# Performance work log

Measured on AMD Instinct MI355X. Metric: run time of the kernel, lower is better.

The kernel has to match this reference:

```python
import jax, jax.numpy as jnp
import numpy as np

K = 2          # diffusion steps
HID = 64       # hidden_dim
T_OUT = 12     # decoder horizon
EPS = 1e-6


def _random_walk(A):
    # W_fwd = D_out^{-1} A ; W_bwd = D_in^{-1} A^T  (row-normalized)
    W_fwd = A / (A.sum(axis=1, keepdims=True) + EPS)
    AT = A.T
    W_bwd = AT / (AT.sum(axis=1, keepdims=True) + EPS)
    return W_fwd, W_bwd


def _dconv(xin, Wf, Wb, W, b):
    # xin: (B, N, F). K forward + K backward random-walk hops, concat, linear.
    outs = [xin]
    xf = xin
    for _ in range(K):
        xf = jnp.einsum('ij,bjf->bif', Wf, xf)
        outs.append(xf)
    xb = xin
    for _ in range(K):
        xb = jnp.einsum('ij,bjf->bif', Wb, xb)
        outs.append(xb)
    return jnp.concatenate(outs, axis=-1) @ W + b


def _cell(xl, h, Wr, br, Wz, bz, Wn, bn, Wf, Wb):
    xh = jnp.concatenate([xl, h], axis=-1)
    r = jax.nn.sigmoid(_dconv(xh, Wf, Wb, Wr, br))
    z = jax.nn.sigmoid(_dconv(xh, Wf, Wb, Wz, bz))
    xrh = jnp.concatenate([xl, r * h], axis=-1)
    n = jnp.tanh(_dconv(xrh, Wf, Wb, Wn, bn))
    return (1.0 - z) * h + z * n


def setup_inputs() -> dict:
    key = jax.random.key(0)
    ks = jax.random.split(key, 20)
    B, T_in, N = 16, 12, 512
    x = jax.random.normal(ks[0], (B, T_in, N), dtype=jnp.float32)
    A = jax.random.uniform(ks[1], (N, N), dtype=jnp.float32)

    def lin(k, fan_in, fan_out):
        s = 1.0 / np.sqrt(fan_in)
        kw, kb = jax.random.split(k)
        W = jax.random.uniform(kw, (fan_in, fan_out), jnp.float32, -s, s)
        b = jax.random.uniform(kb, (fan_out,), jnp.float32, -s, s)
        return W, b

    in0 = (2 * K + 1) * (1 + HID)    # 325
    in1 = (2 * K + 1) * (2 * HID)    # 640
    Wr0, br0 = lin(ks[2], in0, HID)
    Wz0, bz0 = lin(ks[3], in0, HID)
    Wn0, bn0 = lin(ks[4], in0, HID)
    Wr1, br1 = lin(ks[5], in1, HID)
    Wz1, bz1 = lin(ks[6], in1, HID)
    Wn1, bn1 = lin(ks[7], in1, HID)
    Wp, bp = lin(ks[8], HID, 1)
    return dict(x=x, A=A, Wr0=Wr0, br0=br0, Wz0=Wz0, bz0=bz0, Wn0=Wn0, bn0=bn0,
                Wr1=Wr1, br1=br1, Wz1=Wz1, bz1=bz1, Wn1=Wn1, bn1=bn1, Wp=Wp, bp=bp)


def reference(x, A, Wr0, br0, Wz0, bz0, Wn0, bn0,
              Wr1, br1, Wz1, bz1, Wn1, bn1, Wp, bp):
    Wf, Wb = _random_walk(A)
    B, T_in, N = x.shape
    x4 = x[..., None]                             # (B, T_in, N, 1)
    h0 = jnp.zeros((B, N, HID), x.dtype)
    h1 = jnp.zeros((B, N, HID), x.dtype)

    def enc_step(carry, xt):
        h0, h1 = carry
        h0 = _cell(xt, h0, Wr0, br0, Wz0, bz0, Wn0, bn0, Wf, Wb)
        h1 = _cell(h0, h1, Wr1, br1, Wz1, bz1, Wn1, bn1, Wf, Wb)
        return (h0, h1), None

    (h0, h1), _ = jax.lax.scan(enc_step, (h0, h1), jnp.moveaxis(x4, 1, 0))

    def dec_step(carry, _):
        h0, h1, di = carry
        h0 = _cell(di, h0, Wr0, br0, Wz0, bz0, Wn0, bn0, Wf, Wb)
        h1 = _cell(h0, h1, Wr1, br1, Wz1, bz1, Wn1, bn1, Wf, Wb)
        yt = h1 @ Wp + bp                          # (B, N, 1)
        return (h0, h1, yt), yt

    (_, _, _), ys = jax.lax.scan(dec_step, (h0, h1, x4[:, -1]), None, length=T_OUT)
    return jnp.moveaxis(ys, 0, 1)[..., 0]          # (B, T_out, N)
```

## Files before the change

kernel.cpp:

```cpp
#include <hip/hip_runtime.h>
#include <math.h>

#define T_IN   12
#define T_OUT  12
#define NB     8192
#define EPSV   1e-6f

typedef __attribute__((ext_vector_type(8))) short short8;
typedef __attribute__((ext_vector_type(4))) float floatx4;

__device__ __forceinline__ unsigned short f2bf(float x) {
    union { float f; unsigned u; } v; v.f = x;
    unsigned r = v.u + 0x7fffu + ((v.u >> 16) & 1u);
    return (unsigned short)(r >> 16);
}
__device__ __forceinline__ float bf2f(unsigned short h) {
    union { float f; unsigned u; } v; v.u = ((unsigned)h) << 16;
    return v.f;
}
__device__ __forceinline__ unsigned packbf(float v) {
    unsigned u = __float_as_uint(v);
    unsigned hu = u & 0xffff0000u;
    float r = v - __uint_as_float(hu);
    unsigned ru = __float_as_uint(r);
    return (ru & 0xffff0000u) | (u >> 16);
}
__device__ __forceinline__ void split2(float v, short& h, short& l) {
    unsigned u = __float_as_uint(v);
    h = (short)(u >> 16);
    float r = v - __uint_as_float(u & 0xffff0000u);
    l = (short)(__float_as_uint(r) >> 16);
}

__device__ __forceinline__ float sigmoid_fast(float x) {
    return 1.0f / (1.0f + __expf(-x));
}
__device__ __forceinline__ float tanh_fast(float x) {
    float e = __expf(2.0f * x);
    return 1.0f - 2.0f / (e + 1.0f);
}

struct HopA {
    const float* M[4];
    float* dst0[4];
};

struct HopM {
    const unsigned short* Ahi[4]; const unsigned short* Alo[4];
    const unsigned* src0; const unsigned* src1;
    unsigned* dst0[4]; unsigned* dst1[4];
    int tiles0;
};

struct XHopM {
    const unsigned short* Ahi[4]; const unsigned short* Alo[4];
    const float* X;
    float* Y;
    int ncols;
};

struct WPack { const float* w[4]; unsigned short* hi[4]; unsigned short* lo[4]; };

struct Setup {
    const float* A; float* Wf; float* Wb;
    const float* x; float* xenc;
    const float* W[6]; unsigned short* hi[6]; unsigned short* lo[6];
};

struct LinJob {
    const unsigned* seg[10]; int nseg;
    const float* sx[5]; int sxrow[5]; int nsx;
    const unsigned short* Wh[2]; const unsigned short* Wl[2];
    const float* WO[2]; const float* bias[2];
    const float* h; unsigned* GP; float* Z;
    float* PR;
    int mode;
};

struct NJob {
    const unsigned* seg[10]; int nseg; int ksplit;
    const float* sx[5]; int sxrow[5]; int nsx;
    const unsigned short* Wh; const unsigned short* Wl;
    const float* WO; const float* bias;
    const float* Zb; const float* hin; float* hout; unsigned* hPout;
    int doProj; const float* Wp; const float* bp; float* out; float* di; int t;
};

struct F0 {
    const float* M[4];
    const float* di;
    const float* PR;
    const float* WO[2]; const float* bias[2];
    const float* h0;
    unsigned* GP0; float* Z0; float* HXS;
};

__global__ __launch_bounds__(256) void setup_kernel(Setup s) {
    __shared__ float s1[256], s2[256];
    int bx = blockIdx.x;
    int t = threadIdx.x;
    if (bx < 512) {
        int i = bx;
        float a = s.A[i * 512 + t] + s.A[i * 512 + t + 256];
        float b = s.A[t * 512 + i] + s.A[(t + 256) * 512 + i];
        s1[t] = a; s2[t] = b;
        __syncthreads();
        for (int off = 128; off > 0; off >>= 1) {
            if (t < off) { s1[t] += s1[t + off]; s2[t] += s2[t + off]; }
            __syncthreads();
        }
        float irs = 1.0f / (s1[0] + EPSV);
        float ics = 1.0f / (s2[0] + EPSV);
        for (int j = t; j < 512; j += 256) {
            s.Wf[i * 512 + j] = s.A[i * 512 + j] * irs;
            s.Wb[i * 512 + j] = s.A[j * 512 + i] * ics;
        }
    } else if (bx < 896) {
        int idx = (bx - 512) * 256 + t;
        int j = idx & 511;
        int b = (idx >> 9) & 15;
        int tt = idx >> 13;
        s.xenc[tt * NB + j * 16 + b] = s.x[(b * T_IN + tt) * 512 + j];
    } else {
        int bx2 = bx - 896;
        int g = bx2 / 160;
        int nseg = (g < 3) ? 5 : 10;
        int idx = (bx2 % 160) * 256 + t;
        if (idx < nseg * 4096) {
            int j = idx & 7, ln = (idx >> 3) & 15, ntl = (idx >> 7) & 3, O = idx >> 9;
            int sg = O >> 3, o8 = O & 7;
            int base = (g < 3) ? (65 * sg + 1) : (64 * sg);
            int row = base + o8 * 8 + j;
            int col = ntl * 16 + ln;
            float v = s.W[g][(size_t)row * 64 + col];
            unsigned short h = f2bf(v);
            s.hi[g][idx] = h;
            s.lo[g][idx] = f2bf(v - bf2f(h));
        }
    }
}

__global__ __launch_bounds__(256) void ghop_kernel(HopA a) {
    int z = blockIdx.z;
    const float* Wm = a.M[z];
    const float* X = Wm;
    float* Y = a.dst0[z];
    int col0 = blockIdx.x * 64;
    int row0 = blockIdx.y * 64;
    int tid = threadIdx.x;
    int tx = tid & 15, ty = tid >> 4;
    int kkA = tid & 15, rrA = tid >> 4;
    int ccB = tid & 63, kkB = tid >> 6;

    __shared__ float As[16][68], Bs[16][68];
    float acc[4][4] = {};

    const float* wp = Wm + (row0 + rrA) * 512 + kkA;
    const float* xp = X + (size_t)(col0 + ccB) + (size_t)kkB * 512;

    float ra[4], rb[4];
#pragma unroll
    for (int p = 0; p < 4; ++p) ra[p] = wp[p * 16 * 512];
#pragma unroll
    for (int p = 0; p < 4; ++p) rb[p] = xp[(size_t)(p * 4) * 512];

    for (int k0 = 0; k0 < 512; k0 += 16) {
#pragma unroll
        for (int p = 0; p < 4; ++p) As[kkA][rrA + p * 16] = ra[p];
#pragma unroll
        for (int p = 0; p < 4; ++p) Bs[kkB + p * 4][ccB] = rb[p];
        __syncthreads();
        if (k0 + 16 < 512) {
            int kn = k0 + 16;
#pragma unroll
            for (int p = 0; p < 4; ++p) ra[p] = wp[p * 16 * 512 + kn];
#pragma unroll
            for (int p = 0; p < 4; ++p) rb[p] = xp[(size_t)(kn + p * 4) * 512];
        }
#pragma unroll
        for (int k = 0; k < 16; ++k) {
            const float4 a4 = *(const float4*)&As[k][ty * 4];
            const float4 b4 = *(const float4*)&Bs[k][tx * 4];
            float av[4] = { a4.x, a4.y, a4.z, a4.w };
            float bv[4] = { b4.x, b4.y, b4.z, b4.w };
#pragma unroll
            for (int i = 0; i < 4; ++i)
#pragma unroll
                for (int j = 0; j < 4; ++j)
                    acc[i][j] = fmaf(av[i], bv[j], acc[i][j]);
        }
        __syncthreads();
    }

    int colw = col0 + tx * 4;
#pragma unroll
    for (int i = 0; i < 4; ++i) {
        int row = row0 + ty * 4 + i;
        *(float4*)&Y[(size_t)row * 512 + colw] =
            make_float4(acc[i][0], acc[i][1], acc[i][2], acc[i][3]);
    }
}

__global__ void wpack_kernel(WPack a) {
    int z = blockIdx.y;
    int idx = blockIdx.x * 256 + threadIdx.x;
    int m = idx >> 9, k = idx & 511;
    float x = a.w[z][idx];
    unsigned short h = f2bf(x);
    unsigned short l = f2bf(x - bf2f(h));
    int p = (((m >> 4) * 64 + (k >> 3)) * 16 + (m & 15)) * 8 + (k & 7);
    a.hi[z][p] = h;
    a.lo[z][p] = l;
}

template<int MI>
__global__ __launch_bounds__(256) void hop_mfma(HopM a) {
    int z = blockIdx.z;
    int nt = blockIdx.x;
    const unsigned* X; unsigned* Y; int c0;
    if (nt < a.tiles0) { X = a.src0; Y = a.dst0[z]; c0 = nt * 64; }
    else { X = a.src1; Y = a.dst1[z]; c0 = (nt - a.tiles0) * 64; }
    const unsigned short* Ahi = a.Ahi[z];
    const unsigned short* Alo = a.Alo[z];
    int bm = blockIdx.y * (MI * 32);

    __shared__ unsigned short Bhi_s[2][64][40];
    __shared__ unsigned short Blo_s[2][64][40];

    int tid = threadIdx.x;
    int lane = tid & 63, w = tid >> 6;
    int wm = (w & 1) * (MI * 16), wn = (w >> 1) * 32;
    int ln = lane & 15, quad = lane >> 4;
    int sc = tid & 63, skh = tid >> 6;

    floatx4 acc[MI][2];
#pragma unroll
    for (int mi = 0; mi < MI; ++mi)
#pragma unroll
        for (int ci = 0; ci < 2; ++ci) acc[mi][ci] = (floatx4)0.0f;

    const unsigned* xbase = X + c0 + sc;
    int mtb = (bm + wm) >> 4;

    unsigned uv[8];
#pragma unroll
    for (int j = 0; j < 8; ++j)
        uv[j] = xbase[(size_t)(skh * 8 + j) * 1024];
    {
        short8 h8, l8;
#pragma unroll
        for (int j = 0; j < 8; ++j) {
            h8[j] = (short)(uv[j] & 0xffffu);
            l8[j] = (short)(uv[j] >> 16);
        }
        *(short8*)&Bhi_s[0][sc][skh * 8] = h8;
        *(short8*)&Blo_s[0][sc][skh * 8] = l8;
    }
#pragma unroll
    for (int j = 0; j < 8; ++j)
        uv[j] = xbase[(size_t)(32 + skh * 8 + j) * 1024];

    for (int it = 0; it < 16; ++it) {
        __syncthreads();
        int cur = it & 1;
        if (it + 1 < 16) {
            short8 h8, l8;
#pragma unroll
            for (int j = 0; j < 8; ++j) {
                h8[j] = (short)(uv[j] & 0xffffu);
                l8[j] = (short)(uv[j] >> 16);
            }
            *(short8*)&Bhi_s[cur ^ 1][sc][skh * 8] = h8;
            *(short8*)&Blo_s[cur ^ 1][sc][skh * 8] = l8;
        }
        if (it + 2 < 16) {
            int kn = (it + 2) * 32;
#pragma unroll
            for (int j = 0; j < 8; ++j)
                uv[j] = xbase[(size_t)(kn + skh * 8 + j) * 1024];
        }
        short8 bh[2], bl[2];
#pragma unroll
        for (int ci = 0; ci < 2; ++ci) {
            bh[ci] = *(const short8*)&Bhi_s[cur][wn + ci * 16 + ln][quad * 8];
            bl[ci] = *(const short8*)&Blo_s[cur][wn + ci * 16 + ln][quad * 8];
        }
        int kob = it * 4 + quad;
#pragma unroll
        for (int mi = 0; mi < MI; ++mi) {
            size_t aoff = ((size_t)((mtb + mi) * 64 + kob) * 16 + ln) * 8;
            short8 Ah = *(const short8*)(Ahi + aoff);
            short8 Al = *(const short8*)(Alo + aoff);
#pragma unroll
            for (int ci = 0; ci < 2; ++ci) {
                acc[mi][ci] = __builtin_amdgcn_mfma_f32_16x16x32_bf16(Ah, bh[ci], acc[mi][ci], 0, 0, 0);
                acc[mi][ci] = __builtin_amdgcn_mfma_f32_16x16x32_bf16(Ah, bl[ci], acc[mi][ci], 0, 0, 0);
                acc[mi][ci] = __builtin_amdgcn_mfma_f32_16x16x32_bf16(Al, bh[ci], acc[mi][ci], 0, 0, 0);
            }
        }
    }

#pragma unroll
    for (int mi = 0; mi < MI; ++mi) {
#pragma unroll
        for (int ci = 0; ci < 2; ++ci) {
            int mrow = bm + wm + mi * 16 + quad * 4;
            int col = c0 + wn + ci * 16 + ln;
#pragma unroll
            for (int r = 0; r < 4; ++r)
                Y[(size_t)(mrow + r) * 1024 + col] = packbf(acc[mi][ci][r]);
        }
    }
}

__global__ __launch_bounds__(256) void xhop_mfma(XHopM a) {
    int z = blockIdx.z;
    int c0 = blockIdx.x * 64;
    const unsigned short* Ahi = a.Ahi[z];
    const unsigned short* Alo = a.Alo[z];
    int bm = blockIdx.y * 64;

    __shared__ unsigned short Bhi_s[2][64][40];
    __shared__ unsigned short Blo_s[2][64][40];

    int tid = threadIdx.x;
    int lane = tid & 63, w = tid >> 6;
    int wm = (w & 1) * 32, wn = (w >> 1) * 32;
    int ln = lane & 15, quad = lane >> 4;
    int sc = tid & 63, skh = tid >> 6;

    floatx4 acc[2][2];
#pragma unroll
    for (int mi = 0; mi < 2; ++mi)
#pragma unroll
        for (int ci = 0; ci < 2; ++ci) acc[mi][ci] = (floatx4)0.0f;

    int colS = c0 + sc;
    bool ok = colS < a.ncols;
    const float* xb = a.X + (size_t)(colS >> 4) * NB + (colS & 15);
    int mtb = (bm + wm) >> 4;

    float xv[8];
#pragma unroll
    for (int j = 0; j < 8; ++j)
        xv[j] = ok ? xb[(size_t)(skh * 8 + j) * 16] : 0.0f;
    {
        short8 h8, l8;
#pragma unroll
        for (int j = 0; j < 8; ++j) { short h, l; split2(xv[j], h, l); h8[j] = h; l8[j] = l; }
        *(short8*)&Bhi_s[0][sc][skh * 8] = h8;
        *(short8*)&Blo_s[0][sc][skh * 8] = l8;
    }
#pragma unroll
    for (int j = 0; j < 8; ++j)
        xv[j] = ok ? xb[(size_t)(32 + skh * 8 + j) * 16] : 0.0f;

    for (int it = 0; it < 16; ++it) {
        __syncthreads();
        int cur = it & 1;
        if (it + 1 < 16) {
            short8 h8, l8;
#pragma unroll
            for (int j = 0; j < 8; ++j) { short h, l; split2(xv[j], h, l); h8[j] = h; l8[j] = l; }
            *(short8*)&Bhi_s[cur ^ 1][sc][skh * 8] = h8;
            *(short8*)&Blo_s[cur ^ 1][sc][skh * 8] = l8;
        }
        if (it + 2 < 16) {
            int kn = (it + 2) * 32;
#pragma unroll
            for (int j = 0; j < 8; ++j)
                xv[j] = ok ? xb[(size_t)(kn + skh * 8 + j) * 16] : 0.0f;
        }
        short8 bh[2], bl[2];
#pragma unroll
        for (int ci = 0; ci < 2; ++ci) {
            bh[ci] = *(const short8*)&Bhi_s[cur][wn + ci * 16 + ln][quad * 8];
            bl[ci] = *(const short8*)&Blo_s[cur][wn + ci * 16 + ln][quad * 8];
        }
        int kob = it * 4 + quad;
#pragma unroll
        for (int mi = 0; mi < 2; ++mi) {
            size_t aoff = ((size_t)((mtb + mi) * 64 + kob) * 16 + ln) * 8;
            short8 Ah = *(const short8*)(Ahi + aoff);
            short8 Al = *(const short8*)(Alo + aoff);
#pragma unroll
            for (int ci = 0; ci < 2; ++ci) {
                acc[mi][ci] = __builtin_amdgcn_mfma_f32_16x16x32_bf16(Ah, bh[ci], acc[mi][ci], 0, 0, 0);
                acc[mi][ci] = __builtin_amdgcn_mfma_f32_16x16x32_bf16(Ah, bl[ci], acc[mi][ci], 0, 0, 0);
                acc[mi][ci] = __builtin_amdgcn_mfma_f32_16x16x32_bf16(Al, bh[ci], acc[mi][ci], 0, 0, 0);
            }
        }
    }

#pragma unroll
    for (int mi = 0; mi < 2; ++mi) {
#pragma unroll
        for (int ci = 0; ci < 2; ++ci) {
            int col = c0 + wn + ci * 16 + ln;
            if (col < a.ncols) {
                int mrow = bm + wm + mi * 16 + quad * 4;
                float* yb = a.Y + (size_t)((col >> 4) * 4 + z) * NB + (col & 15);
#pragma unroll
                for (int r = 0; r < 4; ++r)
                    yb[(size_t)(mrow + r) * 16] = acc[mi][ci][r];
            }
        }
    }
}

__device__ __forceinline__ void lin_core2(const unsigned* const* segs, int nseg, int s0,
        const unsigned short* __restrict__ Bh, const unsigned short* __restrict__ Bl,
        int row0, int ln, int quad, int cihalf, floatx4 acc[2]) {
    for (int s = 0; s < nseg; ++s) {
        const unsigned* ap = segs[s] + (size_t)(row0 + ln) * 64 + quad * 8;
#pragma unroll
        for (int hh = 0; hh < 2; ++hh) {
            unsigned u[8];
            *(uint4*)&u[0] = *(const uint4*)(ap + hh * 32);
            *(uint4*)&u[4] = *(const uint4*)(ap + hh * 32 + 4);
            short8 Ah, Al;
#pragma unroll
            for (int j = 0; j < 8; ++j) {
                Ah[j] = (short)(u[j] & 0xffffu);
                Al[j] = (short)(u[j] >> 16);
            }
            int O = (s0 + s) * 8 + hh * 4 + quad;
#pragma unroll
            for (int ci = 0; ci < 2; ++ci) {
                int c_abs = cihalf * 2 + ci;
                size_t boff = ((size_t)(O * 4 + c_abs) * 16 + ln) * 8;
                short8 B1 = *(const short8*)(Bh + boff);
                short8 B2 = *(const short8*)(Bl + boff);
                acc[ci] = __builtin_amdgcn_mfma_f32_16x16x32_bf16(Ah, B1, acc[ci], 0, 0, 0);
                acc[ci] = __builtin_amdgcn_mfma_f32_16x16x32_bf16(Al, B1, acc[ci], 0, 0, 0);
                acc[ci] = __builtin_amdgcn_mfma_f32_16x16x32_bf16(Ah, B2, acc[ci], 0, 0, 0);
            }
        }
    }
}

__device__ __forceinline__ void lin_scalar2p(const float* const* sx, const int* sxrow,
        int nsx, const float* __restrict__ WO,
        int row0, int ln, int quad, int cihalf, floatx4 acc[2]) {
    for (int t = 0; t < nsx; ++t) {
        const float* wr = WO + (size_t)sxrow[t] * 64;
        const float* sv = sx[t] + row0 + quad * 4;
#pragma unroll
        for (int rr = 0; rr < 4; ++rr) {
            float v = sv[rr];
#pragma unroll
            for (int ci = 0; ci < 2; ++ci)
                acc[ci][rr] = fmaf(v, wr[(cihalf * 2 + ci) * 16 + ln], acc[ci][rr]);
        }
    }
}

__device__ __forceinline__ void rz_body(const LinJob& J, int bx) {
    int w = threadIdx.x >> 6, lane = threadIdx.x & 63;
    int ln = lane & 15, quad = lane >> 4;
    int row0 = bx * 64 + w * 16;
    int gate = blockIdx.y;
    int cihalf = blockIdx.z;
    floatx4 acc[2];
    acc[0] = (floatx4)0.0f; acc[1] = (floatx4)0.0f;
    lin_core2(J.seg, J.nseg, 0, J.Wh[gate], J.Wl[gate], row0, ln, quad, cihalf, acc);
    if (J.nsx) lin_scalar2p(J.sx, J.sxrow, J.nsx, J.WO[gate], row0, ln, quad, cihalf, acc);
    if (J.mode == 0) {
        const float* bias = J.bias[gate];
#pragma unroll
        for (int ci = 0; ci < 2; ++ci) {
            int col = (cihalf * 2 + ci) * 16 + ln;
            float bv = bias[col];
#pragma unroll
            for (int rr = 0; rr < 4; ++rr) {
                int row = row0 + quad * 4 + rr;
                size_t idx = (size_t)row * 64 + col;
                float sg = sigmoid_fast(acc[ci][rr] + bv);
                if (gate == 0) J.GP[idx] = packbf(sg * J.h[idx]);
                else J.Z[idx] = sg;
            }
        }
    } else {
        float* PRg = J.PR + (size_t)gate * ((size_t)NB * 64);
#pragma unroll
        for (int ci = 0; ci < 2; ++ci) {
            int col = (cihalf * 2 + ci) * 16 + ln;
#pragma unroll
            for (int rr = 0; rr < 4; ++rr) {
                int row = row0 + quad * 4 + rr;
                PRg[(size_t)row * 64 + col] = acc[ci][rr];
            }
        }
    }
}

__global__ __launch_bounds__(256) void lin_rz2(LinJob j0, LinJob j1, int xsplit) {
    if ((int)blockIdx.x >= xsplit) rz_body(j1, (int)blockIdx.x - xsplit);
    else                           rz_body(j0, (int)blockIdx.x);
}

__device__ __forceinline__ void n_body(const NJob& J, int bx) {
    int w = threadIdx.x >> 6, lane = threadIdx.x & 63;
    int ln = lane & 15, quad = lane >> 4;
    int kh = w & 1, cihalf = w >> 1;
    int row0 = bx * 16;
    __shared__ float part[2][2][16][17];
    __shared__ float pr[2][16];
    floatx4 acc[2];
    acc[0] = (floatx4)0.0f; acc[1] = (floatx4)0.0f;
    if (kh == 0) {
        lin_core2(J.seg, J.ksplit, 0, J.Wh, J.Wl, row0, ln, quad, cihalf, acc);
    } else {
        lin_core2(J.seg + J.ksplit, J.nseg - J.ksplit, J.ksplit, J.Wh, J.Wl,
                  row0, ln, quad, cihalf, acc);
        if (J.nsx) lin_scalar2p(J.sx, J.sxrow, J.nsx, J.WO, row0, ln, quad, cihalf, acc);
#pragma unroll
        for (int ci = 0; ci < 2; ++ci)
#pragma unroll
            for (int rr = 0; rr < 4; ++rr)
                part[cihalf][ci][quad * 4 + rr][ln] = acc[ci][rr];
    }
    __syncthreads();
    float p[4] = {0.0f, 0.0f, 0.0f, 0.0f};
    if (kh == 0) {
#pragma unroll
        for (int ci = 0; ci < 2; ++ci) {
            int col = (cihalf * 2 + ci) * 16 + ln;
            float bv = J.bias[col];
            float wpv = J.doProj ? J.Wp[col] : 0.0f;
#pragma unroll
            for (int rr = 0; rr < 4; ++rr) {
                int row = row0 + quad * 4 + rr;
                size_t idx = (size_t)row * 64 + col;
                float pre = acc[ci][rr] + part[cihalf][ci][quad * 4 + rr][ln] + bv;
                float nn = tanh_fast(pre);
                float z = J.Zb[idx];
                float hv = J.hin[idx];
                float o = (1.0f - z) * hv + z * nn;
                J.hout[idx] = o;
                J.hPout[idx] = packbf(o);
                p[rr] = fmaf(o, wpv, p[rr]);
            }
        }
        if (J.doProj) {
#pragma unroll
            for (int rr = 0; rr < 4; ++rr) {
                p[rr] += __shfl_xor(p[rr], 1, 64);
                p[rr] += __shfl_xor(p[rr], 2, 64);
                p[rr] += __shfl_xor(p[rr], 4, 64);
                p[rr] += __shfl_xor(p[rr], 8, 64);
            }
            if (ln == 0) {
#pragma unroll
                for (int rr = 0; rr < 4; ++rr)
                    pr[cihalf][quad * 4 + rr] = p[rr];
            }
        }
    }
    __syncthreads();
    if (J.doProj && kh == 0 && cihalf == 0 && ln == 0) {
        float bpv = J.bp[0];
#pragma unroll
        for (int rr = 0; rr < 4; ++rr) {
            int qr = quad * 4 + rr;
            int row = row0 + qr;
            float y = pr[0][qr] + pr[1][qr] + bpv;
            int n = row >> 4, b = row & 15;
            J.out[(b * T_OUT + J.t) * 512 + n] = y;
            J.di[row] = y;
        }
    }
}

__global__ __launch_bounds__(256) void lin_n2(NJob j0, NJob j1, int xsplit) {
    if ((int)blockIdx.x >= xsplit) n_body(j1, (int)blockIdx.x - xsplit);
    else                           n_body(j0, (int)blockIdx.x);
}

__global__ __launch_bounds__(256) void finish0_kernel(F0 a) {
    int n = blockIdx.x;
    int tid = threadIdx.x;
    __shared__ float hopS[4][16];
    __shared__ float sdi[16];

    int g = tid >> 2;
    int sub = tid & 3;
    int m = g >> 4, b = g & 15;
    const float* wrow = a.M[m] + (size_t)n * 512 + sub * 128;
    const float* dv = a.di + (size_t)(sub * 128) * 16 + b;
    float s0 = 0.0f, s1 = 0.0f, s2 = 0.0f, s3 = 0.0f;
#pragma unroll 8
    for (int k = 0; k < 128; k += 4) {
        float4 w4 = *(const float4*)&wrow[k];
        s0 = fmaf(w4.x, dv[(k + 0) * 16], s0);
        s1 = fmaf(w4.y, dv[(k + 1) * 16], s1);
        s2 = fmaf(w4.z, dv[(k + 2) * 16], s2);
        s3 = fmaf(w4.w, dv[(k + 3) * 16], s3);
    }
    float sv = (s0 + s1) + (s2 + s3);
    sv += __shfl_xor(sv, 1, 64);
    sv += __shfl_xor(sv, 2, 64);
    if (sub == 0) {
        hopS[m][b] = sv;
        a.HXS[(size_t)m * NB + n * 16 + b] = sv;
    }
    if (tid < 16) sdi[tid] = a.di[n * 16 + tid];
    __syncthreads();

    int gate = tid >> 7, col = tid & 63, rh = (tid >> 6) & 1;
    const float* WOg = a.WO[gate];
    float w0c = WOg[col];
    float wmc[4];
#pragma unroll
    for (int mm = 0; mm < 4; ++mm)
        wmc[mm] = WOg[(size_t)(65 * (mm + 1)) * 64 + col];
    float bv = a.bias[gate][col];
    const float* PRg = a.PR + (size_t)gate * ((size_t)NB * 64);
#pragma unroll
    for (int rr = 0; rr < 8; ++rr) {
        int bl = rh * 8 + rr;
        int row = n * 16 + bl;
        size_t idx = (size_t)row * 64 + col;
        float pre = PRg[idx] + bv + sdi[bl] * w0c;
#pragma unroll
        for (int mm = 0; mm < 4; ++mm)
            pre = fmaf(hopS[mm][bl], wmc[mm], pre);
        float sg = sigmoid_fast(pre);
        if (gate == 0) a.GP0[idx] = packbf(sg * a.h0[idx]);
        else a.Z0[idx] = sg;
    }
}

extern "C" void kernel_launch(void* const* d_in, const int* in_sizes, int n_in,
                              void* d_out, int out_size, void* d_ws, size_t ws_size,
                              hipStream_t stream) {
    (void)in_sizes; (void)n_in; (void)out_size; (void)ws_size;
    const float* x   = (const float*)d_in[0];
    const float* A   = (const float*)d_in[1];
    const float* Wr0 = (const float*)d_in[2];  const float* br0 = (const float*)d_in[3];
    const float* Wz0 = (const float*)d_in[4];  const float* bz0 = (const float*)d_in[5];
    const float* Wn0 = (const float*)d_in[6];  const float* bn0 = (const float*)d_in[7];
    const float* Wr1 = (const float*)d_in[8];  const float* br1 = (const float*)d_in[9];
    const float* Wz1 = (const float*)d_in[10]; const float* bz1 = (const float*)d_in[11];
    const float* Wn1 = (const float*)d_in[12]; const float* bn1 = (const float*)d_in[13];
    const float* Wp  = (const float*)d_in[14]; const float* bp  = (const float*)d_in[15];
    float* out = (float*)d_out;

    float* ws = (float*)d_ws;
    size_t off = 0;
    auto alloc = [&](size_t nf) { float* p = ws + off; off += nf; return p; };
    const size_t NB64 = (size_t)NB * 64;
    float* Wf  = alloc(262144); float* Wb  = alloc(262144);
    float* W2f = alloc(262144); float* W2b = alloc(262144);
    float* xenc = alloc((size_t)T_IN * NB);
    unsigned short* Whi[4]; unsigned short* Wlo[4];
    for (int m = 0; m < 4; ++m) Whi[m] = (unsigned short*)alloc(131072);
    for (int m = 0; m < 4; ++m) Wlo[m] = (unsigned short*)alloc(131072);
    float* zbase = alloc(12 * NB64);
    float* h0x[2]; unsigned* h0Px[2];
    h0x[1]  = zbase;
    h0Px[1] = (unsigned*)(zbase + NB64);
    float* h1 = zbase + 2 * NB64;
    unsigned* h1P = (unsigned*)(zbase + 3 * NB64);
    unsigned* HAall = (unsigned*)(zbase + 4 * NB64);
    unsigned* HBall = (unsigned*)(zbase + 8 * NB64);
    unsigned* HA[4]; unsigned* HB[4]; unsigned* HG0[4]; unsigned* HG1[4];
    for (int m = 0; m < 4; ++m) HA[m] = HAall + m * NB64;
    for (int m = 0; m < 4; ++m) HB[m] = HBall + m * NB64;
    for (int m = 0; m < 4; ++m) HG0[m] = (unsigned*)alloc(NB64);
    for (int m = 0; m < 4; ++m) HG1[m] = (unsigned*)alloc(NB64);
    unsigned* GP0 = (unsigned*)alloc(NB64);
    unsigned* GP1 = (unsigned*)alloc(NB64);
    float* Z0 = alloc(NB64);
    float* Z1 = alloc(NB64);
    h0x[0]  = alloc(NB64);
    h0Px[0] = (unsigned*)alloc(NB64);
    float* PR0 = alloc(2 * NB64);
    float* XHE = alloc((size_t)T_IN * 4 * NB);
    float* HXSdec = alloc(4 * NB);
    float* di = alloc(NB);
    unsigned short* LWh[6]; unsigned short* LWl[6];
    for (int g = 0; g < 3; ++g) { LWh[g] = (unsigned short*)alloc(10240); LWl[g] = (unsigned short*)alloc(10240); }
    for (int g = 3; g < 6; ++g) { LWh[g] = (unsigned short*)alloc(20480); LWl[g] = (unsigned short*)alloc(20480); }

    hipMemsetAsync(zbase, 0, 12 * NB64 * 4, stream);

    {
        Setup s;
        s.A = A; s.Wf = Wf; s.Wb = Wb;
        s.x = x; s.xenc = xenc;
        const float* WG[6] = { Wr0, Wz0, Wn0, Wr1, Wz1, Wn1 };
        for (int g = 0; g < 6; ++g) { s.W[g] = WG[g]; s.hi[g] = LWh[g]; s.lo[g] = LWl[g]; }
        setup_kernel<<<dim3(1856), 256, 0, stream>>>(s);
    }
    {
        HopA w2 = {};
        w2.M[0] = Wf; w2.M[1] = Wb;
        w2.dst0[0] = W2f; w2.dst0[1] = W2b;
        ghop_kernel<<<dim3(8, 8, 2), 256, 0, stream>>>(w2);
    }
    {
        WPack p;
        p.w[0] = Wf; p.w[1] = W2f; p.w[2] = Wb; p.w[3] = W2b;
        for (int m = 0; m < 4; ++m) { p.hi[m] = Whi[m]; p.lo[m] = Wlo[m]; }
        wpack_kernel<<<dim3(1024, 4), 256, 0, stream>>>(p);
    }
    {
        XHopM xa = {};
        for (int m = 0; m < 4; ++m) { xa.Ahi[m] = Whi[m]; xa.Alo[m] = Wlo[m]; }
        xa.X = xenc; xa.Y = XHE; xa.ncols = 192;
        xhop_mfma<<<dim3(3, 8, 4), 256, 0, stream>>>(xa);
    }

    auto hopSingle = [&](const unsigned* s0, unsigned* const* d0) {
        HopM a = {};
        for (int m = 0; m < 4; ++m) { a.Ahi[m] = Whi[m]; a.Alo[m] = Wlo[m]; }
        a.src0 = s0; a.tiles0 = 16;
        for (int m = 0; m < 4; ++m) a.dst0[m] = d0[m];
        hop_mfma<1><<<dim3(16, 16, 4), 256, 0, stream>>>(a);
    };
    auto hopDual = [&](const unsigned* s0, unsigned* const* d0,
                       const unsigned* s1, unsigned* const* d1) {
        HopM a = {};
        for (int m = 0; m < 4; ++m) { a.Ahi[m] = Whi[m]; a.Alo[m] = Wlo[m]; }
        a.src0 = s0; a.tiles0 = 16;
        for (int m = 0; m < 4; ++m) a.dst0[m] = d0[m];
        a.src1 = s1;
        for (int m = 0; m < 4; ++m) a.dst1[m] = d1[m];
        hop_mfma<2><<<dim3(32, 8, 4), 256, 0, stream>>>(a);
    };

    auto mkRZ1 = [&](int t) {
        LinJob J = {};
        J.seg[0] = h0Px[t & 1]; J.seg[1] = h1P;
        for (int m = 0; m < 4; ++m) { J.seg[2 + 2 * m] = HA[m]; J.seg[3 + 2 * m] = HB[m]; }
        J.nseg = 10; J.nsx = 0;
        J.Wh[0] = LWh[3]; J.Wl[0] = LWl[3]; J.Wh[1] = LWh[4]; J.Wl[1] = LWl[4];
        J.WO[0] = Wr1; J.WO[1] = Wz1; J.bias[0] = br1; J.bias[1] = bz1;
        J.h = h1; J.GP = GP1; J.Z = Z1; J.mode = 0;
        return J;
    };
    auto mkRZ0 = [&](int tn, const float* xc, const float* hx, int mode) {
        LinJob J = {};
        J.seg[0] = h0Px[(tn - 1) & 1];
        for (int m = 0; m < 4; ++m) J.seg[1 + m] = HA[m];
        J.nseg = 5;
        if (mode == 0) {
            J.nsx = 5;
            J.sx[0] = xc; J.sxrow[0] = 0;
            for (int m = 0; m < 4; ++m) { J.sx[1 + m] = hx + (size_t)m * NB; J.sxrow[1 + m] = 65 * (m + 1); }
        }
        J.Wh[0] = LWh[0]; J.Wl[0] = LWl[0]; J.Wh[1] = LWh[1]; J.Wl[1] = LWl[1];
        J.WO[0] = Wr0; J.WO[1] = Wz0; J.bias[0] = br0; J.bias[1] = bz0;
        J.h = h0x[(tn - 1) & 1]; J.GP = GP0; J.Z = Z0; J.PR = PR0; J.mode = mode;
        return J;
    };
    auto mkN1 = [&](int t) {
        NJob J = {};
        J.seg[0] = h0Px[t & 1]; J.seg[1] = GP1;
        for (int m = 0; m < 4; ++m) { J.seg[2 + 2 * m] = HA[m]; J.seg[3 + 2 * m] = HG1[m]; }
        J.nseg = 10; J.ksplit = 5; J.nsx = 0;
        J.Wh = LWh[5]; J.Wl = LWl[5]; J.WO = Wn1; J.bias = bn1;
        J.Zb = Z1; J.hin = h1; J.hout = h1; J.hPout = h1P;
        J.doProj = (t >= T_IN); J.Wp = Wp; J.bp = bp; J.out = out; J.di = di; J.t = t - T_IN;
        return J;
    };
    auto mkN0 = [&](int tn, const float* xc, const float* hx) {
        NJob J = {};
        J.seg[0] = GP0;
        for (int m = 0; m < 4; ++m) J.seg[1 + m] = HG0[m];
        J.nseg = 5; J.ksplit = 3;
        J.nsx = 5;
        J.sx[0] = xc; J.sxrow[0] = 0;
        for (int m = 0; m < 4; ++m) { J.sx[1 + m] = hx + (size_t)m * NB; J.sxrow[1 + m] = 65 * (m + 1); }
        J.Wh = LWh[2]; J.Wl = LWl[2]; J.WO = Wn0; J.bias = bn0;
        J.Zb = Z0; J.hin = h0x[(tn - 1) & 1]; J.hout = h0x[tn & 1]; J.hPout = h0Px[tn & 1];
        J.doProj = 0;
        return J;
    };

    auto rz2one = [&](LinJob a) { lin_rz2<<<dim3(128, 2, 2), 256, 0, stream>>>(a, a, 128); };
    auto rz2two = [&](LinJob a, LinJob b) { lin_rz2<<<dim3(256, 2, 2), 256, 0, stream>>>(a, b, 128); };
    auto n2one = [&](NJob a) { lin_n2<<<dim3(512), 256, 0, stream>>>(a, a, 512); };
    auto n2two = [&](NJob a, NJob b) { lin_n2<<<dim3(1024), 256, 0, stream>>>(a, b, 512); };

    rz2one(mkRZ0(0, xenc, XHE, 0));
    hopSingle(GP0, HG0);
    n2one(mkN0(0, xenc, XHE));
    hopSingle(h0Px[0], HA);

    for (int t = 0; t < T_IN + T_OUT; ++t) {
        int tn = t + 1;
        bool last = (t == T_IN + T_OUT - 1);
        bool decFeed = (tn >= T_IN + 1);
        if (!last && !decFeed) {
            int ts = (tn < T_IN) ? tn : (T_IN - 1);
            const float* xc = xenc + (size_t)ts * NB;
            const float* hx = XHE + (size_t)ts * 4 * NB;
            rz2two(mkRZ1(t), mkRZ0(tn, xc, hx, 0));
            hopDual(GP1, HG1, GP0, HG0);
            n2two(mkN1(t), mkN0(tn, xc, hx));
            hopDual(h0Px[tn & 1], HA, h1P, HB);
        } else if (!last) {
            rz2two(mkRZ1(t), mkRZ0(tn, nullptr, nullptr, 1));
            hopSingle(GP1, HG1);
            n2one(mkN1(t));
            {
                F0 f = {};
                f.M[0] = Wf; f.M[1] = W2f; f.M[2] = Wb; f.M[3] = W2b;
                f.di = di; f.PR = PR0;
                f.WO[0] = Wr0; f.WO[1] = Wz0; f.bias[0] = br0; f.bias[1] = bz0;
                f.h0 = h0x[t & 1];
                f.GP0 = GP0; f.Z0 = Z0; f.HXS = HXSdec;
                finish0_kernel<<<dim3(512), 256, 0, stream>>>(f);
            }
            hopSingle(GP0, HG0);
            n2one(mkN0(tn, di, HXSdec));
            hopDual(h0Px[tn & 1], HA, h1P, HB);
        } else {
            rz2one(mkRZ1(t));
            hopSingle(GP1, HG1);
            n2one(mkN1(t));
        }
    }
}
```

Before: 2.708 ms.

## Share staged hop input across paired diffusion matrices in one block

Replaces the per-matrix hop kernel with one where each block computes two propagation matrices (e.g. W and W^2) against the same staged B tile. This halves the global loads and LDS conversions of the input columns per matrix pair and halves the z grid dimension. In exchange each warp holds two matrices' worth of accumulators and A loads per iteration. For the dual case the M tile per block is no longer doubled, so the A reuse that the old MI=2 tiling gave is traded for B reuse.

Measured after the change: 2.782 ms. 2.7% more time.

```diff
diff --git a/kernel.cpp b/kernel.cpp
--- a/kernel.cpp
+++ b/kernel.cpp
@@ -213,34 +213,39 @@
     a.lo[z][p] = l;
 }
 
-template<int MI>
-__global__ __launch_bounds__(256) void hop_mfma(HopM a) {
-    int z = blockIdx.z;
+__global__ __launch_bounds__(256) void hopz_mfma(HopM a) {
+    int zp = blockIdx.z;
     int nt = blockIdx.x;
-    const unsigned* X; unsigned* Y; int c0;
-    if (nt < a.tiles0) { X = a.src0; Y = a.dst0[z]; c0 = nt * 64; }
-    else { X = a.src1; Y = a.dst1[z]; c0 = (nt - a.tiles0) * 64; }
-    const unsigned short* Ahi = a.Ahi[z];
-    const unsigned short* Alo = a.Alo[z];
-    int bm = blockIdx.y * (MI * 32);
+    const unsigned* X; unsigned* Y0; unsigned* Y1; int c0;
+    if (nt < a.tiles0) {
+        X = a.src0; Y0 = a.dst0[2 * zp]; Y1 = a.dst0[2 * zp + 1]; c0 = nt * 64;
+    } else {
+        X = a.src1; Y0 = a.dst1[2 * zp]; Y1 = a.dst1[2 * zp + 1];
+        c0 = (nt - a.tiles0) * 64;
+    }
+    const unsigned short* Ahi0 = a.Ahi[2 * zp];
+    const unsigned short* Alo0 = a.Alo[2 * zp];
+    const unsigned short* Ahi1 = a.Ahi[2 * zp + 1];
+    const unsigned short* Alo1 = a.Alo[2 * zp + 1];
+    int bm = blockIdx.y * 32;
 
     __shared__ unsigned short Bhi_s[2][64][40];
     __shared__ unsigned short Blo_s[2][64][40];
 
     int tid = threadIdx.x;
     int lane = tid & 63, w = tid >> 6;
-    int wm = (w & 1) * (MI * 16), wn = (w >> 1) * 32;
+    int wm = (w & 1) * 16, wn = (w >> 1) * 32;
     int ln = lane & 15, quad = lane >> 4;
     int sc = tid & 63, skh = tid >> 6;
-
-    floatx4 acc[MI][2];
-#pragma unroll
-    for (int mi = 0; mi < MI; ++mi)
-#pragma unroll
-        for (int ci = 0; ci < 2; ++ci) acc[mi][ci] = (floatx4)0.0f;
+    int mtb = (bm + wm) >> 4;
+
+    floatx4 acc[2][2];
+#pragma unroll
+    for (int zz = 0; zz < 2; ++zz)
+#pragma unroll
+        for (int ci = 0; ci < 2; ++ci) acc[zz][ci] = (floatx4)0.0f;
 
     const unsigned* xbase = X + c0 + sc;
-    int mtb = (bm + wm) >> 4;
 
     unsigned uv[8];
 #pragma unroll
@@ -286,29 +291,32 @@
             bl[ci] = *(const short8*)&Blo_s[cur][wn + ci * 16 + ln][quad * 8];
         }
         int kob = it * 4 + quad;
-#pragma unroll
-        for (int mi = 0; mi < MI; ++mi) {
-            size_t aoff = ((size_t)((mtb + mi) * 64 + kob) * 16 + ln) * 8;
-            short8 Ah = *(const short8*)(Ahi + aoff);
-            short8 Al = *(const short8*)(Alo + aoff);
-#pragma unroll
-            for (int ci = 0; ci < 2; ++ci) {
-                acc[mi][ci] = __builtin_amdgcn_mfma_f32_16x16x32_bf16(Ah, bh[ci], acc[mi][ci], 0, 0, 0);
-                acc[mi][ci] = __builtin_amdgcn_mfma_f32_16x16x32_bf16(Ah, bl[ci], acc[mi][ci], 0, 0, 0);
-                acc[mi][ci] = __builtin_amdgcn_mfma_f32_16x16x32_bf16(Al, bh[ci], acc[mi][ci], 0, 0, 0);
-            }
-        }
-    }
-
-#pragma unroll
-    for (int mi = 0; mi < MI; ++mi) {
+        size_t aoff = ((size_t)(mtb * 64 + kob) * 16 + ln) * 8;
+        short8 A0h = *(const short8*)(Ahi0 + aoff);
+        short8 A0l = *(const short8*)(Alo0 + aoff);
+        short8 A1h = *(const short8*)(Ahi1 + aoff);
+        short8 A1l = *(const short8*)(Alo1 + aoff);
 #pragma unroll
         for (int ci = 0; ci < 2; ++ci) {
-            int mrow = bm + wm + mi * 16 + quad * 4;
+            acc[0][ci] = __builtin_amdgcn_mfma_f32_16x16x32_bf16(A0h, bh[ci], acc[0][ci], 0, 0, 0);
+            acc[0][ci] = __builtin_amdgcn_mfma_f32_16x16x32_bf16(A0h, bl[ci], acc[0][ci], 0, 0, 0);
+            acc[0][ci] = __builtin_amdgcn_mfma_f32_16x16x32_bf16(A0l, bh[ci], acc[0][ci], 0, 0, 0);
+            acc[1][ci] = __builtin_amdgcn_mfma_f32_16x16x32_bf16(A1h, bh[ci], acc[1][ci], 0, 0, 0);
+            acc[1][ci] = __builtin_amdgcn_mfma_f32_16x16x32_bf16(A1h, bl[ci], acc[1][ci], 0, 0, 0);
+            acc[1][ci] = __builtin_amdgcn_mfma_f32_16x16x32_bf16(A1l, bh[ci], acc[1][ci], 0, 0, 0);
+        }
+    }
+
+#pragma unroll
+    for (int zz = 0; zz < 2; ++zz) {
+        unsigned* Y = zz ? Y1 : Y0;
+#pragma unroll
+        for (int ci = 0; ci < 2; ++ci) {
+            int mrow = bm + wm + quad * 4;
             int col = c0 + wn + ci * 16 + ln;
 #pragma unroll
             for (int r = 0; r < 4; ++r)
-                Y[(size_t)(mrow + r) * 1024 + col] = packbf(acc[mi][ci][r]);
+                Y[(size_t)(mrow + r) * 1024 + col] = packbf(acc[zz][ci][r]);
         }
     }
 }
@@ -717,7 +725,7 @@
         for (int m = 0; m < 4; ++m) { a.Ahi[m] = Whi[m]; a.Alo[m] = Wlo[m]; }
         a.src0 = s0; a.tiles0 = 16;
         for (int m = 0; m < 4; ++m) a.dst0[m] = d0[m];
-        hop_mfma<1><<<dim3(16, 16, 4), 256, 0, stream>>>(a);
+        hopz_mfma<<<dim3(16, 16, 2), 256, 0, stream>>>(a);
     };
     auto hopDual = [&](const unsigned* s0, unsigned* const* d0,
                        const unsigned* s1, unsigned* const* d1) {
@@ -727,7 +735,7 @@
         for (int m = 0; m < 4; ++m) a.dst0[m] = d0[m];
         a.src1 = s1;
         for (int m = 0; m < 4; ++m) a.dst1[m] = d1[m];
-        hop_mfma<2><<<dim3(32, 8, 4), 256, 0, stream>>>(a);
+        hopz_mfma<<<dim3(32, 16, 2), 256, 0, stream>>>(a);
     };
 
     auto mkRZ1 = [&](int t) {
```
